# Optimization experiments

Measured on AMD Instinct MI355X. Metric: run time of the kernel, lower is better.

## Reference

```python
import jax, jax.numpy as jnp
import numpy as np


def _lstm_dir(x, w_ih, w_hh, b_ih, b_hh, reverse):
    # x: [B, L, D]; w_ih: [4H, D]; w_hh: [4H, H]; PyTorch gate order i,f,g,o
    B = x.shape[0]
    H = w_hh.shape[1]
    h0 = jnp.zeros((B, H), x.dtype)

    def cell(carry, x_t):
        h, c = carry
        z = x_t @ w_ih.T + h @ w_hh.T + b_ih + b_hh
        i, f, g, o = jnp.split(z, 4, axis=-1)
        c = jax.nn.sigmoid(f) * c + jax.nn.sigmoid(i) * jnp.tanh(g)
        h = jax.nn.sigmoid(o) * jnp.tanh(c)
        return (h, c), h

    _, hs = jax.lax.scan(cell, (h0, h0), jnp.swapaxes(x, 0, 1), reverse=reverse)
    return jnp.swapaxes(hs, 0, 1)  # [B, L, H]


def setup_inputs() -> dict:
    key = jax.random.key(0)
    ks = jax.random.split(key, 16)
    B, L, V, D, H, E, A = 32, 128, 30000, 300, 128, 34, 36
    s = 0.05
    rn = lambda k, shape: jax.random.normal(k, shape, jnp.float32) * s
    return {
        "input_ids": jax.random.randint(ks[0], (B, L), 0, V),
        "emb": rn(ks[1], (V, D)),
        "w_ih_f": rn(ks[2], (4 * H, D)), "w_hh_f": rn(ks[3], (4 * H, H)),
        "b_ih_f": rn(ks[4], (4 * H,)), "b_hh_f": rn(ks[5], (4 * H,)),
        "w_ih_b": rn(ks[6], (4 * H, D)), "w_hh_b": rn(ks[7], (4 * H, H)),
        "b_ih_b": rn(ks[8], (4 * H,)), "b_hh_b": rn(ks[9], (4 * H,)),
        "event_w": rn(ks[10], (E, 2 * H)), "event_b": rn(ks[11], (E,)),
        "arg_w": rn(ks[12], (A, 4 * H + E - 1)), "arg_b": rn(ks[13], (A,)),
    }


def reference(input_ids, emb, w_ih_f, w_hh_f, b_ih_f, b_hh_f,
              w_ih_b, w_hh_b, b_ih_b, b_hh_b,
              event_w, event_b, arg_w, arg_b):
    # Eval mode: dropout is identity. No labels -> return (event_logits, arguments_logits).
    B, L = input_ids.shape
    E = event_b.shape[0]
    x = emb[input_ids]  # [B, L, D]
    h_f = _lstm_dir(x, w_ih_f, w_hh_f, b_ih_f, b_hh_f, False)
    h_b = _lstm_dir(x, w_ih_b, w_hh_b, b_ih_b, b_hh_b, True)
    hidden = jnp.concatenate([h_f, h_b], axis=-1)  # [B, L, 2H]
    col_range = jnp.arange(E - 1)
    g0 = jnp.zeros((B, L, E - 1), hidden.dtype)  # running g_trg_arg memory

    def step(g, h_i):  # h_i: [B, 2H] = trigger hidden state at timestep i
        ev_logit = h_i @ event_w.T + event_b  # [B, E]
        ev_pred = jnp.argmax(ev_logit, axis=-1)  # [B]
        trig = jnp.broadcast_to(h_i[:, None, :], hidden.shape)  # [B, L, 2H]
        ah = jnp.concatenate([hidden, trig, g], axis=-1)  # [B, L, 4H+E-1]
        arg_logit = ah @ arg_w.T + arg_b  # [B, L, A]
        arg_pred = jnp.argmax(arg_logit, axis=-1)  # [B, L]
        # Vectorized update_g_trg_arg: for batch items with ev_pred>0, set
        # column (ev_pred-1) to 1 wherever arg_pred>0, else keep previous value.
        mask_ev = ev_pred > 0  # [B]
        col = jnp.where(mask_ev, ev_pred - 1, 0)  # [B]
        onehot = (col[:, None] == col_range[None, :]) & mask_ev[:, None]  # [B, E-1]
        cond = onehot[:, None, :] & (arg_pred[:, :, None] > 0)  # [B, L, E-1]
        g = jnp.where(cond, jnp.ones((), g.dtype), g)
        return g, (ev_logit, arg_logit)

    _, (ev_logits, arg_logits) = jax.lax.scan(step, g0, jnp.swapaxes(hidden, 0, 1))
    event_logits = jnp.swapaxes(ev_logits, 0, 1)  # [B, L, E]
    arguments_logits = jnp.swapaxes(arg_logits, 0, 1)  # [B, L, L, A]
    return event_logits, arguments_logits
```

## Files before the change

### kernel.cpp

```cpp
#include <hip/hip_runtime.h>
#include <hip/hip_bf16.h>
#include <stdint.h>

#define B_  32
#define L_  128
#define D_  300
#define DP_ 304
#define H_  128
#define G_  512
#define E_  34
#define A_  36
#define M_  4096
#define NC_ 106
#define NCP 112
#define CH_ 8
#define NCH 16
#define LCH 8

__device__ __forceinline__ float sigf(float x){ return 1.0f / (1.0f + expf(-x)); }

__global__ void k_prep1(const float* __restrict__ wihf, const float* __restrict__ wihb,
                        float* __restrict__ WT){
    int k = blockIdx.x;
    int d = blockIdx.y;
    int n = threadIdx.x;
    const float* w = d ? wihb : wihf;
    WT[((size_t)d * DP_ + k) * G_ + n] = (k < D_) ? w[(size_t)n * D_ + k] : 0.0f;
}

__global__ void k_prep2(const float* __restrict__ evw, const float* __restrict__ evb,
                        const float* __restrict__ argw, const float* __restrict__ argb,
                        float* __restrict__ WcatT, float* __restrict__ biasv){
    int k = blockIdx.x;
    int n = threadIdx.x;
    if (n >= NCP) return;
    float v = 0.0f;
    if (n < E_)       v = evw[(size_t)n * 256 + k];
    else if (n < 70)  v = argw[(size_t)(n - 34) * 545 + k];
    else if (n < NC_) v = argw[(size_t)(n - 70) * 545 + 256 + k];
    WcatT[(size_t)k * NCP + n] = v;
    if (k == 0){
        float bv = 0.0f;
        if (n < E_) bv = evb[n];
        else if (n < 70) bv = argb[n - 34];
        biasv[n] = bv;
    }
}

__launch_bounds__(256)
__global__ void k_gemm1(const int* __restrict__ ids, const float* __restrict__ emb,
                        const float* __restrict__ WT,
                        const float* __restrict__ bihf, const float* __restrict__ bhhf,
                        const float* __restrict__ bihb, const float* __restrict__ bhhb,
                        float* __restrict__ XW){
    __shared__ __align__(16) float xs[DP_][8];
    int d  = blockIdx.y;
    int m0 = blockIdx.x * 8;
    int tid = threadIdx.x;
    for (int idx = tid; idx < 8 * DP_; idx += 256){
        int r = idx / DP_, k = idx % DP_;
        int id = ids[m0 + r];
        xs[k][r] = (k < D_) ? emb[(size_t)id * D_ + k] : 0.0f;
    }
    __syncthreads();
    int n0 = tid, n1 = tid + 256;
    const float* w0 = WT + (size_t)d * DP_ * G_ + n0;
    const float* w1 = WT + (size_t)d * DP_ * G_ + n1;
    const float4* xs4 = (const float4*)xs;
    float acc0[8] = {}, acc1[8] = {};
    #pragma unroll 2
    for (int k = 0; k < D_; k++){
        float wv0 = w0[(size_t)k * G_];
        float wv1 = w1[(size_t)k * G_];
        float4 xA = xs4[k * 2], xB = xs4[k * 2 + 1];
        acc0[0] += xA.x * wv0; acc0[1] += xA.y * wv0;
        acc0[2] += xA.z * wv0; acc0[3] += xA.w * wv0;
        acc0[4] += xB.x * wv0; acc0[5] += xB.y * wv0;
        acc0[6] += xB.z * wv0; acc0[7] += xB.w * wv0;
        acc1[0] += xA.x * wv1; acc1[1] += xA.y * wv1;
        acc1[2] += xA.z * wv1; acc1[3] += xA.w * wv1;
        acc1[4] += xB.x * wv1; acc1[5] += xB.y * wv1;
        acc1[6] += xB.z * wv1; acc1[7] += xB.w * wv1;
    }
    float bias0 = d ? (bihb[n0] + bhhb[n0]) : (bihf[n0] + bhhf[n0]);
    float bias1 = d ? (bihb[n1] + bhhb[n1]) : (bihf[n1] + bhhf[n1]);
    for (int r = 0; r < 8; r++){
        XW[((size_t)d * M_ + m0 + r) * G_ + n0] = acc0[r] + bias0;
        XW[((size_t)d * M_ + m0 + r) * G_ + n1] = acc1[r] + bias1;
    }
}

#define STEP(S_, XWV)                                                           \
{                                                                               \
    float a0=0.f,a1=0.f,a2=0.f,a3=0.f;                                          \
    _Pragma("unroll")                                                           \
    for (int q = 0; q < 16; q++){                                               \
        float4 hv = hc[q];                                                      \
        a0 += wv[q].x * hv.x; a1 += wv[q].y * hv.y;                             \
        a2 += wv[q].z * hv.z; a3 += wv[q].w * hv.w;                             \
    }                                                                           \
    float part  = (a0 + a1) + (a2 + a3);                                        \
    float other = __shfl_xor(part, 1);                                          \
    if (half == 0){                                                             \
        float z = ((XWV) + part) + other;                                       \
        zbuf[row] = gate_g ? tanhf(z) : sigf(z);                                \
    }                                                                           \
    __syncthreads();                                                            \
    if (pb){                                                                    \
        float I = zbuf[tid], F = zbuf[H_ + tid];                                \
        float G = zbuf[2*H_ + tid], O = zbuf[3*H_ + tid];                       \
        c = F * c + I * G;                                                      \
        float h = O * tanhf(c);                                                 \
        hball[tid] = h; hball[132 + tid] = h;                                   \
        hist[(size_t)(S_) * H_ + tid] = h;                                      \
    }                                                                           \
    __syncthreads();                                                            \
}

__launch_bounds__(1024, 2)
__global__ void k_lstm(const float* __restrict__ XW, const float* __restrict__ whhf,
                       const float* __restrict__ whhb, float* __restrict__ Hid){
    __shared__ __align__(16) float hball[260];
    __shared__ float zbuf[G_];
    __shared__ __align__(16) float hist[L_ * H_];
    int bid = blockIdx.x;
    int d = bid >> 5, b = bid & 31;
    int tid = threadIdx.x;
    int row = tid >> 1;
    int half = tid & 1;
    bool gate_g = (row >= 256) && (row < 384);
    bool pb = (tid < H_);
    const float* whh = d ? whhb : whhf;
    const float4* wr = (const float4*)(whh + (size_t)row * H_ + half * 64);
    float4 wv[16];
    #pragma unroll
    for (int q = 0; q < 16; q++) wv[q] = wr[q];
    const float4* hc = (const float4*)(hball + (half ? 196 : 0));
    float c = 0.0f;
    if (tid < H_){ hball[tid] = 0.0f; hball[132 + tid] = 0.0f; }
    __syncthreads();
    const float* xwn = XW + ((size_t)d * M_ + (size_t)b * L_) * G_ + row;
    #pragma unroll 1
    for (int ch = 0; ch < L_ / LCH; ch++){
        float xr[LCH];
        #pragma unroll
        for (int j = 0; j < LCH; j++){
            int s_ = ch * LCH + j;
            int t_ = d ? (L_ - 1 - s_) : s_;
            xr[j] = xwn[(size_t)t_ * G_];
        }
        #pragma unroll
        for (int j = 0; j < LCH; j++){
            STEP(ch * LCH + j, xr[j])
        }
    }
    const float4* hist4 = (const float4*)hist;
    #pragma unroll
    for (int q = 0; q < 4; q++){
        int idx = tid + q * 1024;
        int sl = idx >> 5, n4 = idx & 31;
        int t_ = d ? (L_ - 1 - sl) : sl;
        *(float4*)(Hid + ((size_t)b * L_ + t_) * 256 + d * H_ + n4 * 4) =
            hist4[(size_t)sl * 32 + n4];
    }
}

__launch_bounds__(128)
__global__ void k_heads2(const float* __restrict__ Hid, const float* __restrict__ WcatT,
                         const float* __restrict__ biasv,
                         float* __restrict__ out0, float* __restrict__ Base,
                         float* __restrict__ T2, int* __restrict__ Evcol){
    __shared__ float hs[256];
    __shared__ float evl[E_];
    int m = blockIdx.x;
    int tid = threadIdx.x;
    hs[tid]       = Hid[(size_t)m * 256 + tid];
    hs[tid + 128] = Hid[(size_t)m * 256 + 128 + tid];
    __syncthreads();
    float acc = 0.0f;
    if (tid < NC_){
        const float* wc = WcatT + tid;
        for (int k = 0; k < 256; k++) acc += hs[k] * wc[(size_t)k * NCP];
        acc += biasv[tid];
    }
    if (tid < E_){
        out0[(size_t)m * E_ + tid] = acc;
        evl[tid] = acc;
    } else if (tid < 70){
        Base[(size_t)m * A_ + (tid - 34)] = acc;
    } else if (tid < NC_){
        T2[(size_t)m * A_ + (tid - 70)] = acc;
    }
    __syncthreads();
    if (tid == 0){
        float best = evl[0]; int bi = 0;
        for (int e = 1; e < E_; e++){
            float v = evl[e];
            if (v > best){ best = v; bi = e; }
        }
        Evcol[m] = bi - 1;
    }
}

__launch_bounds__(128)
__global__ void k_scan1(const float* __restrict__ Base, const float* __restrict__ T2,
                        const int* __restrict__ Evcol, const float* __restrict__ argw,
                        float* __restrict__ Snap, uint64_t* __restrict__ MaskSnap){
    __shared__ float t2s[L_ * A_];
    __shared__ float wgs[33 * A_];
    __shared__ int   evc[L_];
    int b = blockIdx.x;
    int l = threadIdx.x;
    for (int idx = l; idx < L_ * A_; idx += 128)
        t2s[idx] = T2[(size_t)b * L_ * A_ + idx];
    for (int idx = l; idx < 33 * A_; idx += 128){
        int c = idx / A_, a = idx % A_;
        wgs[idx] = argw[(size_t)a * 545 + 512 + c];
    }
    evc[l] = Evcol[b * L_ + l];
    __syncthreads();
    float bg[A_];
    {
        const float* bp = Base + ((size_t)b * L_ + l) * A_;
        #pragma unroll
        for (int a = 0; a < A_; a++) bg[a] = bp[a];
    }
    uint64_t mask = 0;
    #pragma unroll 1
    for (int i = 0; i < L_; i++){
        if ((i & (CH_ - 1)) == 0){
            int ch = i >> 3;
            float* sp = Snap + (((size_t)b * NCH + ch) * L_ + l) * A_;
            #pragma unroll
            for (int a = 0; a < A_; a++) sp[a] = bg[a];
            MaskSnap[((size_t)b * NCH + ch) * L_ + l] = mask;
        }
        const float* tr = t2s + i * A_;
        float lg0 = bg[0] + tr[0];
        float m1  = bg[1] + tr[1];
        #pragma unroll
        for (int a = 2; a < A_; a++) m1 = fmaxf(m1, bg[a] + tr[a]);
        bool apos = m1 > lg0;
        int cc = evc[i];
        if (cc >= 0 && apos && !((mask >> cc) & 1ull)){
            mask |= 1ull << cc;
            const float* wc = wgs + cc * A_;
            #pragma unroll
            for (int a = 0; a < A_; a++) bg[a] += wc[a];
        }
    }
}

__launch_bounds__(128)
__global__ void k_scan2(const float* __restrict__ T2, const int* __restrict__ Evcol,
                        const float* __restrict__ argw,
                        const float* __restrict__ Snap, const uint64_t* __restrict__ MaskSnap,
                        float* __restrict__ argout){
    __shared__ float t2s[CH_ * A_];
    __shared__ float wgs[33 * A_];
    __shared__ int   evc[CH_];
    int ch = blockIdx.x;
    int b  = blockIdx.y;
    int l  = threadIdx.x;
    int i0 = ch * CH_;
    for (int idx = l; idx < CH_ * A_; idx += 128)
        t2s[idx] = T2[((size_t)b * L_ + i0) * A_ + idx];
    for (int idx = l; idx < 33 * A_; idx += 128){
        int c = idx / A_, a = idx % A_;
        wgs[idx] = argw[(size_t)a * 545 + 512 + c];
    }
    if (l < CH_) evc[l] = Evcol[b * L_ + i0 + l];
    __syncthreads();
    float bg[A_];
    {
        const float* sp = Snap + (((size_t)b * NCH + ch) * L_ + l) * A_;
        #pragma unroll
        for (int a = 0; a < A_; a++) bg[a] = sp[a];
    }
    uint64_t mask = MaskSnap[((size_t)b * NCH + ch) * L_ + l];
    #pragma unroll 1
    for (int s = 0; s < CH_; s++){
        int i = i0 + s;
        const float* tr = t2s + s * A_;
        float lg[A_];
        #pragma unroll
        for (int a = 0; a < A_; a++) lg[a] = bg[a] + tr[a];
        float m1 = lg[1];
        #pragma unroll
        for (int a = 2; a < A_; a++) m1 = fmaxf(m1, lg[a]);
        bool apos = m1 > lg[0];
        float* op = argout + (((size_t)b * L_ + i) * L_ + l) * A_;
        #pragma unroll
        for (int q = 0; q < 9; q++){
            float4 v; v.x = lg[4*q]; v.y = lg[4*q+1]; v.z = lg[4*q+2]; v.w = lg[4*q+3];
            *(float4*)(op + 4 * q) = v;
        }
        int cc = evc[s];
        if (cc >= 0 && apos && !((mask >> cc) & 1ull)){
            mask |= 1ull << cc;
            const float* wc = wgs + cc * A_;
            #pragma unroll
            for (int a = 0; a < A_; a++) bg[a] += wc[a];
        }
    }
}

extern "C" void kernel_launch(void* const* d_in, const int* in_sizes, int n_in,
                              void* d_out, int out_size, void* d_ws, size_t ws_size,
                              hipStream_t stream){
    const int*   ids  = (const int*)  d_in[0];
    const float* emb  = (const float*)d_in[1];
    const float* wihf = (const float*)d_in[2];
    const float* whhf = (const float*)d_in[3];
    const float* bihf = (const float*)d_in[4];
    const float* bhhf = (const float*)d_in[5];
    const float* wihb = (const float*)d_in[6];
    const float* whhb = (const float*)d_in[7];
    const float* bihb = (const float*)d_in[8];
    const float* bhhb = (const float*)d_in[9];
    const float* evw  = (const float*)d_in[10];
    const float* evb  = (const float*)d_in[11];
    const float* argw = (const float*)d_in[12];
    const float* argb = (const float*)d_in[13];

    float* out0   = (float*)d_out;
    float* argout = out0 + (size_t)M_ * E_;

    char* w = (char*)d_ws;
    float* WT    = (float*)w; w += (size_t)2 * DP_ * G_ * 4;
    float* XW    = (float*)w; w += (size_t)2 * M_ * G_ * 4;
    float* Hid   = (float*)w; w += (size_t)M_ * 256 * 4;
    float* WcatT = (float*)w; w += (size_t)256 * NCP * 4;
    float* biasv = (float*)w; w += (size_t)NCP * 4;
    float* Base  = (float*)w; w += (size_t)M_ * A_ * 4;
    float* T2    = (float*)w; w += (size_t)M_ * A_ * 4;
    int*   Evcol = (int*)w;   w += (size_t)M_ * 4;

    float*    Snap     = XW;
    uint64_t* MaskSnap = (uint64_t*)(XW + (size_t)B_ * NCH * L_ * A_);

    k_prep1<<<dim3(DP_, 2), 512, 0, stream>>>(wihf, wihb, WT);
    k_prep2<<<256, 128, 0, stream>>>(evw, evb, argw, argb, WcatT, biasv);
    k_gemm1<<<dim3(M_ / 8, 2), 256, 0, stream>>>(ids, emb, WT, bihf, bhhf, bihb, bhhb, XW);
    k_lstm<<<64, 1024, 0, stream>>>(XW, whhf, whhb, Hid);
    k_heads2<<<M_, 128, 0, stream>>>(Hid, WcatT, biasv, out0, Base, T2, Evcol);
    k_scan1<<<B_, 128, 0, stream>>>(Base, T2, Evcol, argw, Snap, MaskSnap);
    k_scan2<<<dim3(NCH, B_), 128, 0, stream>>>(T2, Evcol, argw, Snap, MaskSnap, argout);
}
```

Before: 392.9 us.

## Restructure LSTM recurrence to one thread per gate row with wave-shuffle gate exchange

The LSTM kernel moves from 1024 threads (two threads per gate row, a shared-memory gate buffer, and two barriers per step) to 512 threads with one full gate row per thread. Each wave holds the i/f/g/o rows of 16 hidden units, so the gates are exchanged with lane shuffles and each timestep needs only one barrier. The hidden state is double-buffered in shared memory, and the next 8-step chunk of input projections is prefetched while the current chunk runs. In exchange, each thread keeps 128 recurrent weights in registers, which raises register pressure, and the dot product per step is twice as long.

```diff
diff --git a/kernel.cpp b/kernel.cpp
--- a/kernel.cpp
+++ b/kernel.cpp
@@ -16,6 +16,7 @@
 #define CH_ 8
 #define NCH 16
 #define LCH 8
+#define NCHK (L_ / LCH)
 
 __device__ __forceinline__ float sigf(float x){ return 1.0f / (1.0f + expf(-x)); }
 
@@ -90,74 +91,83 @@
     }
 }
 
-#define STEP(S_, XWV)                                                           \
+#define PF(XR, CHI)                                                             \
 {                                                                               \
-    float a0=0.f,a1=0.f,a2=0.f,a3=0.f;                                          \
+    if ((CHI) < NCHK){                                                          \
+        _Pragma("unroll")                                                       \
+        for (int j = 0; j < LCH; j++){                                          \
+            int s_ = (CHI) * LCH + j;                                           \
+            int t_ = d ? (L_ - 1 - s_) : s_;                                    \
+            XR[j] = xwn[(size_t)t_ * G_];                                       \
+        }                                                                       \
+    }                                                                           \
+}
+
+#define STEP8(XR, CHI)                                                          \
+{                                                                               \
     _Pragma("unroll")                                                           \
-    for (int q = 0; q < 16; q++){                                               \
-        float4 hv = hc[q];                                                      \
-        a0 += wv[q].x * hv.x; a1 += wv[q].y * hv.y;                             \
-        a2 += wv[q].z * hv.z; a3 += wv[q].w * hv.w;                             \
+    for (int j = 0; j < LCH; j++){                                              \
+        int s_ = (CHI) * LCH + j;                                               \
+        const float4* hc = (const float4*)((j & 1) ? hb1 : hb0);                \
+        float a0=0.f,a1=0.f,a2=0.f,a3=0.f;                                      \
+        _Pragma("unroll")                                                       \
+        for (int q = 0; q < 32; q++){                                           \
+            float4 hv = hc[q];                                                  \
+            a0 += wv[q].x * hv.x; a1 += wv[q].y * hv.y;                         \
+            a2 += wv[q].z * hv.z; a3 += wv[q].w * hv.w;                         \
+        }                                                                       \
+        float z = XR[j] + ((a0 + a1) + (a2 + a3));                              \
+        float v = (gi == 2) ? tanhf(z) : sigf(z);                               \
+        float Fv = __shfl_xor(v, 16);                                           \
+        float Gv = __shfl_xor(v, 32);                                           \
+        float Ov = __shfl_xor(v, 48);                                           \
+        if (lane < 16){                                                         \
+            c = Fv * c + v * Gv;                                                \
+            float h = Ov * tanhf(c);                                            \
+            float* hw = (j & 1) ? hb0 : hb1;                                    \
+            hw[n16] = h;                                                        \
+            hist[(size_t)(s_) * H_ + n16] = h;                                  \
+        }                                                                       \
+        __syncthreads();                                                        \
     }                                                                           \
-    float part  = (a0 + a1) + (a2 + a3);                                        \
-    float other = __shfl_xor(part, 1);                                          \
-    if (half == 0){                                                             \
-        float z = ((XWV) + part) + other;                                       \
-        zbuf[row] = gate_g ? tanhf(z) : sigf(z);                                \
-    }                                                                           \
-    __syncthreads();                                                            \
-    if (pb){                                                                    \
-        float I = zbuf[tid], F = zbuf[H_ + tid];                                \
-        float G = zbuf[2*H_ + tid], O = zbuf[3*H_ + tid];                       \
-        c = F * c + I * G;                                                      \
-        float h = O * tanhf(c);                                                 \
-        hball[tid] = h; hball[132 + tid] = h;                                   \
-        hist[(size_t)(S_) * H_ + tid] = h;                                      \
-    }                                                                           \
-    __syncthreads();                                                            \
-}
-
-__launch_bounds__(1024, 2)
+}
+
+__launch_bounds__(512, 2)
 __global__ void k_lstm(const float* __restrict__ XW, const float* __restrict__ whhf,
                        const float* __restrict__ whhb, float* __restrict__ Hid){
-    __shared__ __align__(16) float hball[260];
-    __shared__ float zbuf[G_];
+    __shared__ __align__(16) float hb0[H_];
+    __shared__ __align__(16) float hb1[H_];
     __shared__ __align__(16) float hist[L_ * H_];
     int bid = blockIdx.x;
     int d = bid >> 5, b = bid & 31;
     int tid = threadIdx.x;
-    int row = tid >> 1;
-    int half = tid & 1;
-    bool gate_g = (row >= 256) && (row < 384);
-    bool pb = (tid < H_);
+    int wvi  = tid >> 6;
+    int lane = tid & 63;
+    int n16  = wvi * 16 + (lane & 15);
+    int gi   = lane >> 4;
+    int row  = gi * H_ + n16;
     const float* whh = d ? whhb : whhf;
-    const float4* wr = (const float4*)(whh + (size_t)row * H_ + half * 64);
-    float4 wv[16];
+    const float4* wr = (const float4*)(whh + (size_t)row * H_);
+    float4 wv[32];
     #pragma unroll
-    for (int q = 0; q < 16; q++) wv[q] = wr[q];
-    const float4* hc = (const float4*)(hball + (half ? 196 : 0));
+    for (int q = 0; q < 32; q++) wv[q] = wr[q];
     float c = 0.0f;
-    if (tid < H_){ hball[tid] = 0.0f; hball[132 + tid] = 0.0f; }
+    if (tid < H_) hb0[tid] = 0.0f;
     __syncthreads();
     const float* xwn = XW + ((size_t)d * M_ + (size_t)b * L_) * G_ + row;
+    float xA[LCH], xB[LCH];
+    PF(xA, 0)
     #pragma unroll 1
-    for (int ch = 0; ch < L_ / LCH; ch++){
-        float xr[LCH];
-        #pragma unroll
-        for (int j = 0; j < LCH; j++){
-            int s_ = ch * LCH + j;
-            int t_ = d ? (L_ - 1 - s_) : s_;
-            xr[j] = xwn[(size_t)t_ * G_];
-        }
-        #pragma unroll
-        for (int j = 0; j < LCH; j++){
-            STEP(ch * LCH + j, xr[j])
-        }
+    for (int cp = 0; cp < NCHK / 2; cp++){
+        PF(xB, 2 * cp + 1)
+        STEP8(xA, 2 * cp)
+        PF(xA, 2 * cp + 2)
+        STEP8(xB, 2 * cp + 1)
     }
     const float4* hist4 = (const float4*)hist;
     #pragma unroll
-    for (int q = 0; q < 4; q++){
-        int idx = tid + q * 1024;
+    for (int q = 0; q < 8; q++){
+        int idx = tid + q * 512;
         int sl = idx >> 5, n4 = idx & 31;
         int t_ = d ? (L_ - 1 - sl) : sl;
         *(float4*)(Hid + ((size_t)b * L_ + t_) * 256 + d * H_ + n4 * 4) =
@@ -342,7 +352,7 @@
     k_prep1<<<dim3(DP_, 2), 512, 0, stream>>>(wihf, wihb, WT);
     k_prep2<<<256, 128, 0, stream>>>(evw, evb, argw, argb, WcatT, biasv);
     k_gemm1<<<dim3(M_ / 8, 2), 256, 0, stream>>>(ids, emb, WT, bihf, bhhf, bihb, bhhb, XW);
-    k_lstm<<<64, 1024, 0, stream>>>(XW, whhf, whhb, Hid);
+    k_lstm<<<64, 512, 0, stream>>>(XW, whhf, whhb, Hid);
     k_heads2<<<M_, 128, 0, stream>>>(Hid, WcatT, biasv, out0, Base, T2, Evcol);
     k_scan1<<<B_, 128, 0, stream>>>(Base, T2, Evcol, argw, Snap, MaskSnap);
     k_scan2<<<dim3(NCH, B_), 128, 0, stream>>>(T2, Evcol, argw, Snap, MaskSnap, argout);
```

Measured after the change: 392.4 us. No clear change (-0.1%).
